# Kernel optimization log

Measured on AMD Instinct MI355X. Metric: run time of the kernel, lower is better.

Reference implementation:

```python
import jax, jax.numpy as jnp
import numpy as np

WS = 7        # window_size
HEADS = 4     # dim_in // dim_head = 256 // 64
DH = 64       # dim_head (for q/k)
SCALE = DH ** -0.5


def setup_inputs() -> dict:
    key = jax.random.key(0)
    k1, k2, k3 = jax.random.split(key, 3)
    x = jax.random.normal(k1, (32, 256, 56, 56), dtype=jnp.float32)
    qk_w = jax.random.normal(k2, (512, 256), dtype=jnp.float32) * 0.02  # 1x1 conv: (out_c, in_c)
    v_w = jax.random.normal(k3, (256, 256), dtype=jnp.float32) * 0.02
    return {"x": x, "qk_w": qk_w, "v_w": v_w}


def _forward(x, qk_w, v_w):
    B, C, H, W = x.shape
    pad_b = (WS - H % WS) % WS
    pad_r = (WS - W % WS) % WS
    x = jnp.pad(x, ((0, 0), (0, 0), (0, pad_b), (0, pad_r)))
    Hp, Wp = H + pad_b, W + pad_r
    n1, n2 = Hp // WS, Wp // WS

    # 1x1 convs (no bias): qk -> 2*C channels, v -> dim_mid channels with ReLU
    qk = jnp.einsum('bchw,oc->bohw', x, qk_w)
    v = jax.nn.relu(jnp.einsum('bchw,oc->bohw', x, v_w))

    # remote (dilated grid) partition: 'b c (h1 n1) (w1 n2) -> (b n1 n2) c h1 w1'
    def part_r(t):
        b, c = t.shape[:2]
        return t.reshape(b, c, WS, n1, WS, n2).transpose(0, 3, 5, 1, 2, 4).reshape(b * n1 * n2, c, WS, WS)

    def merge_r(t, b):
        c = t.shape[1]
        return t.reshape(b, n1, n2, c, WS, WS).transpose(0, 3, 4, 1, 5, 2).reshape(b, c, Hp, Wp)

    # close (contiguous window) partition: 'b c (n1 h1) (n2 w1) -> (b n1 n2) c h1 w1'
    def part_c(t):
        b, c = t.shape[:2]
        return t.reshape(b, c, n1, WS, n2, WS).transpose(0, 2, 4, 1, 3, 5).reshape(b * n1 * n2, c, WS, WS)

    def merge_c(t, b):
        c = t.shape[1]
        return t.reshape(b, n1, n2, c, WS, WS).transpose(0, 3, 1, 4, 2, 5).reshape(b, c, Hp, Wp)

    def win_attn(qk_win, v_win):
        # qk_win: (bw, 2*HEADS*DH, WS, WS); channel order is (qk, heads, dim_head)
        bw = qk_win.shape[0]
        N = WS * WS
        qkr = qk_win.reshape(bw, 2, HEADS, DH, N)
        q = qkr[:, 0].transpose(0, 1, 3, 2)  # (bw, heads, N, DH)
        k = qkr[:, 1].transpose(0, 1, 3, 2)
        dhv = v_win.shape[1] // HEADS
        vv = v_win.reshape(bw, HEADS, dhv, N).transpose(0, 1, 3, 2)  # (bw, heads, N, dhv)
        attn = jax.nn.softmax(jnp.einsum('bhnd,bhmd->bhnm', q, k) * SCALE, axis=-1)
        o = jnp.einsum('bhnm,bhmd->bhnd', attn, vv)
        return o.transpose(0, 1, 3, 2).reshape(bw, HEADS * dhv, WS, WS)

    o_remote = merge_r(win_attn(part_r(qk), part_r(v)), B)
    o_close = merge_c(win_attn(part_c(qk), part_c(v)), B)
    out = o_remote + o_close
    return out[:, :, :H, :W]


def reference(x, qk_w, v_w):
    return _forward(x, qk_w, v_w)
```

## Files before the change

### kernel.cpp

```cpp
#include <hip/hip_runtime.h>
#include <stdint.h>


typedef float f32x4 __attribute__((ext_vector_type(4)));
typedef __attribute__((ext_vector_type(8))) short short8;

union V16 { uint4 u; short8 s; unsigned short h[8]; };

typedef const __attribute__((address_space(1))) uint32_t* gp_t;
typedef __attribute__((address_space(3))) uint32_t* lp_t;

__device__ __forceinline__ void async16(const void* g, void* l) {
  __builtin_amdgcn_global_load_lds((gp_t)g, (lp_t)l, 16, 0, 0);
}

__device__ __forceinline__ unsigned short f2bf(float f) {
  union { float f; uint32_t u; } a; a.f = f;
  uint32_t u = a.u;
  return (unsigned short)((u + 0x7FFFu + ((u >> 16) & 1u)) >> 16);
}

__device__ __forceinline__ unsigned short f2bf_rhu(float f) {
  union { float f; uint32_t u; } a; a.f = f;
  return (unsigned short)((a.u + 0x8000u) >> 16);
}

__device__ __forceinline__ float bf2f(uint32_t bits_hi16) {
  union { uint32_t u; float f; } a; a.u = bits_hi16; return a.f;
}

__global__ __launch_bounds__(256) void k_wconv(const float* __restrict__ qk_w,
                                               const float* __restrict__ v_w,
                                               unsigned short* __restrict__ Wb) {
  int i = blockIdx.x * 256 + threadIdx.x;
  int o = i >> 5, gidx = i & 31;
  int c0 = gidx * 8;
  const float* src = (o < 512) ? (qk_w + o * 256 + c0) : (v_w + (o - 512) * 256 + c0);
  unsigned short vv[8];
#pragma unroll
  for (int j = 0; j < 8; j++) vv[j] = f2bf(src[j]);
  uint4 u;
  u.x = (uint32_t)vv[0] | ((uint32_t)vv[1] << 16);
  u.y = (uint32_t)vv[2] | ((uint32_t)vv[3] << 16);
  u.z = (uint32_t)vv[4] | ((uint32_t)vv[5] << 16);
  u.w = (uint32_t)vv[6] | ((uint32_t)vv[7] << 16);
  int kb = gidx >> 3, gg = gidx & 7;
  char* dst = (char*)Wb + (size_t)o * 512 + kb * 128 + ((gg ^ (o & 7)) << 4);
  *(uint4*)dst = u;
}

__global__ __launch_bounds__(256) void k_xpose(const float* __restrict__ x,
                                               unsigned short* __restrict__ xT) {
  const int t = threadIdx.x;
  const int p = blockIdx.x * 64 + (t >> 2);
  const int sub = t & 3;
  const int c0 = blockIdx.y * 32 + sub * 8;
  const int b = blockIdx.z;
  const float* xp = x + ((size_t)(b * 256 + c0)) * 3136 + p;
  unsigned short vv[8];
#pragma unroll
  for (int j = 0; j < 8; j++) vv[j] = f2bf(xp[(size_t)j * 3136]);
  uint4 u;
  u.x = (uint32_t)vv[0] | ((uint32_t)vv[1] << 16);
  u.y = (uint32_t)vv[2] | ((uint32_t)vv[3] << 16);
  u.z = (uint32_t)vv[4] | ((uint32_t)vv[5] << 16);
  u.w = (uint32_t)vv[6] | ((uint32_t)vv[7] << 16);
  const int g = (c0 >> 3) & 7;
  const int kb = c0 >> 6;
  char* dst = (char*)xT + ((size_t)(b * 3136 + p)) * 512 + kb * 128 + ((g ^ (p & 7)) << 4);
  *(uint4*)dst = u;
}

__global__ __launch_bounds__(256) void k_conv(const unsigned short* __restrict__ Wb,
                                              const unsigned short* __restrict__ xT,
                                              unsigned short* __restrict__ qkv) {
  __shared__ uint4 lds4[2048];
  char* ldsA = (char*)lds4;
  char* ldsB = (char*)lds4 + 16384;
  const int bi = blockIdx.x;
  const int xcd = bi & 7, g = bi >> 3;
  const int bgrp = g / 150;
  const int rem = g - bgrp * 150;
  const int b = xcd + 8 * bgrp;
  const int ot = rem / 25;
  const int pt = rem - ot * 25;
  const int p0 = pt * 128, o0 = ot * 128;
  const bool isv = (ot >= 4);
  const float qs = (ot < 2) ? 0.18033688011112042f : 1.0f;

  const int tid = threadIdx.x;
  const int lane = tid & 63, wave = tid >> 6;
  const int lid = lane & 15, quad = lane >> 4;
  const int m_off = (wave & 1) * 64, n_off = (wave >> 1) * 64;
  const int psub = lane >> 3, chunk = lane & 7;
  const size_t rowb = (size_t)(b * 3136 + p0);
  const char* xTb = (const char*)xT;
  const char* Wbb = (const char*)Wb;

  f32x4 acc[4][4];
#pragma unroll
  for (int mi = 0; mi < 4; mi++)
#pragma unroll
    for (int ni = 0; ni < 4; ni++) { f32x4 z = {0.f, 0.f, 0.f, 0.f}; acc[mi][ni] = z; }

  for (int kk = 0; kk < 256; kk += 64) {
#pragma unroll
    for (int r = 0; r < 4; r++) {
      int i = wave * 4 + r;
      const char* ga = Wbb + (size_t)(o0 + i * 8 + psub) * 512 + kk * 2 + chunk * 16;
      async16(ga, ldsA + i * 1024);
      const char* gb = xTb + (rowb + i * 8 + psub) * 512 + kk * 2 + chunk * 16;
      async16(gb, ldsB + i * 1024);
    }
    __syncthreads();

    V16 a[4][2], bf[4][2];
#pragma unroll
    for (int mi = 0; mi < 4; mi++) {
      int ro = m_off + mi * 16 + lid;
#pragma unroll
      for (int ks = 0; ks < 2; ks++) {
        int gl = ks * 4 + quad;
        a[mi][ks].u = *(const uint4*)(ldsA + ro * 128 + ((gl ^ (ro & 7)) << 4));
      }
    }
#pragma unroll
    for (int ni = 0; ni < 4; ni++) {
      int px = n_off + ni * 16 + lid;
#pragma unroll
      for (int ks = 0; ks < 2; ks++) {
        int gl = ks * 4 + quad;
        bf[ni][ks].u = *(const uint4*)(ldsB + px * 128 + ((gl ^ (px & 7)) << 4));
      }
    }
#pragma unroll
    for (int mi = 0; mi < 4; mi++)
#pragma unroll
      for (int ni = 0; ni < 4; ni++) {
        acc[mi][ni] = __builtin_amdgcn_mfma_f32_16x16x32_bf16(a[mi][0].s, bf[ni][0].s, acc[mi][ni], 0, 0, 0);
        acc[mi][ni] = __builtin_amdgcn_mfma_f32_16x16x32_bf16(a[mi][1].s, bf[ni][1].s, acc[mi][ni], 0, 0, 0);
      }
    __syncthreads();
  }

#pragma unroll
  for (int mi = 0; mi < 4; mi++) {
    int o = o0 + m_off + mi * 16 + quad * 4;
#pragma unroll
    for (int ni = 0; ni < 4; ni++) {
      int px = p0 + n_off + ni * 16 + lid;
      if (px < 3136) {
        f32x4 v = acc[mi][ni];
        v.x *= qs; v.y *= qs; v.z *= qs; v.w *= qs;
        if (isv) {
          v.x = fmaxf(v.x, 0.f); v.y = fmaxf(v.y, 0.f);
          v.z = fmaxf(v.z, 0.f); v.w = fmaxf(v.w, 0.f);
        }
        ushort4 u;
        u.x = f2bf(v.x); u.y = f2bf(v.y); u.z = f2bf(v.z); u.w = f2bf(v.w);
        *(ushort4*)(qkv + ((size_t)(b * 3136 + px)) * 768 + o) = u;
      }
    }
  }
}

__global__ __launch_bounds__(256) void k_attn(const unsigned short* __restrict__ qkv,
                                              unsigned short* __restrict__ oR,
                                              unsigned short* __restrict__ oC) {
  __shared__ uint4 smem4[2048];
  const int bi = blockIdx.x;
  const int xcd = bi & 7, g = bi >> 3;
  const int b = ((g >> 7) << 3) + xcd;
  const int rem = g & 127;
  const int part = rem >> 6;
  const int w = rem & 63;
  const int i1 = w >> 3, i2 = w & 7;
  const int off = part ? (i1 * 392 + i2 * 7) : (i1 * 56 + i2);
  const int sh  = part ? 56 : 448;
  const int sw  = part ? 1 : 8;

  const int lane = threadIdx.x & 63;
  const int head = threadIdx.x >> 6;
  const int lid = lane & 15, quad = lane >> 4;
  char* Pb = (char*)smem4 + head * 8192;
  const unsigned short* __restrict__ qkvb = qkv + (size_t)b * 3136 * 768;
  unsigned short* __restrict__ oSb = (part ? oC : oR) + (size_t)b * 3136 * 256;

  auto pix = [&](int t) -> int {
    int h1 = (t * 37) >> 8;
    int w1 = t - h1 * 7;
    return off + h1 * sh + w1 * sw;
  };

  V16 va[4][2];
#pragma unroll
  for (int ks = 0; ks < 2; ks++)
#pragma unroll
    for (int j = 0; j < 8; j++) {
      int key = ks * 32 + quad * 8 + j;
      int p = pix(min(key, 48));
      const unsigned short* vp = qkvb + p * 768 + 512 + head * 64 + lid;
#pragma unroll
      for (int mi = 0; mi < 4; mi++) va[mi][ks].h[j] = vp[mi * 16];
    }

  V16 qf[4][2], kf[4][2];
#pragma unroll
  for (int mi = 0; mi < 4; mi++) {
    int p = pix(min(mi * 16 + lid, 48));
    const unsigned short* qp = qkvb + p * 768 + head * 64;
#pragma unroll
    for (int ks = 0; ks < 2; ks++) qf[mi][ks].u = *(const uint4*)(qp + ks * 32 + quad * 8);
  }
#pragma unroll
  for (int ni = 0; ni < 4; ni++) {
    int p = pix(min(ni * 16 + lid, 48));
    const unsigned short* kp = qkvb + p * 768 + 256 + head * 64;
#pragma unroll
    for (int ks = 0; ks < 2; ks++) kf[ni][ks].u = *(const uint4*)(kp + ks * 32 + quad * 8);
  }

  f32x4 s[4][4];
#pragma unroll
  for (int mi = 0; mi < 4; mi++)
#pragma unroll
    for (int ni = 0; ni < 4; ni++) {
      f32x4 z = {0.f, 0.f, 0.f, 0.f};
      z = __builtin_amdgcn_mfma_f32_16x16x32_bf16(qf[mi][0].s, kf[ni][0].s, z, 0, 0, 0);
      z = __builtin_amdgcn_mfma_f32_16x16x32_bf16(qf[mi][1].s, kf[ni][1].s, z, 0, 0, 0);
      s[mi][ni] = z;
    }

  bool kvalid[4];
#pragma unroll
  for (int ni = 0; ni < 4; ni++) kvalid[ni] = (ni * 16 + lid) < 49;
  const int cl2 = (lid & 7) * 2;
#pragma unroll
  for (int mi = 0; mi < 4; mi++) {
#pragma unroll
    for (int r = 0; r < 4; r++) {
      int row = mi * 16 + quad * 4 + r;
      char* rp = Pb + row * 128;
      int rx = row & 7;
#pragma unroll
      for (int ni = 0; ni < 4; ni++) {
        float t = kvalid[ni] ? __builtin_amdgcn_exp2f(s[mi][ni][r]) : 0.f;
        int colgrp = ni * 2 + (lid >> 3);
        *(unsigned short*)(rp + (((colgrp ^ rx) << 4) + cl2)) = f2bf_rhu(t);
      }
    }
  }
  __syncthreads();

  V16 pt[4][2];
#pragma unroll
  for (int ni = 0; ni < 4; ni++) {
    int row = ni * 16 + lid;
#pragma unroll
    for (int ks = 0; ks < 2; ks++) {
      int gl = ks * 4 + quad;
      pt[ni][ks].u = *(const uint4*)(Pb + row * 128 + ((gl ^ (row & 7)) << 4));
    }
  }

  V16 ones;
#pragma unroll
  for (int j = 0; j < 8; j++) ones.h[j] = 0x3F80;
  float inv[4];
  int pq[4]; bool qv[4];
#pragma unroll
  for (int ni = 0; ni < 4; ni++) {
    f32x4 z = {0.f, 0.f, 0.f, 0.f};
    z = __builtin_amdgcn_mfma_f32_16x16x32_bf16(ones.s, pt[ni][0].s, z, 0, 0, 0);
    z = __builtin_amdgcn_mfma_f32_16x16x32_bf16(ones.s, pt[ni][1].s, z, 0, 0, 0);
    inv[ni] = __builtin_amdgcn_rcpf(z[0]);
    int q = ni * 16 + lid;
    qv[ni] = q < 49;
    pq[ni] = pix(qv[ni] ? q : 48);
  }

#pragma unroll
  for (int mi = 0; mi < 4; mi++) {
    f32x4 om[4];
#pragma unroll
    for (int ni = 0; ni < 4; ni++) {
      f32x4 z = {0.f, 0.f, 0.f, 0.f};
      z = __builtin_amdgcn_mfma_f32_16x16x32_bf16(va[mi][0].s, pt[ni][0].s, z, 0, 0, 0);
      z = __builtin_amdgcn_mfma_f32_16x16x32_bf16(va[mi][1].s, pt[ni][1].s, z, 0, 0, 0);
      om[ni] = z;
    }
#pragma unroll
    for (int ni = 0; ni < 4; ni++) {
      if (qv[ni]) {
        float iv = inv[ni];
        uint32_t lo = ((uint32_t)f2bf_rhu(om[ni][0] * iv)) | ((uint32_t)f2bf_rhu(om[ni][1] * iv) << 16);
        uint32_t hi = ((uint32_t)f2bf_rhu(om[ni][2] * iv)) | ((uint32_t)f2bf_rhu(om[ni][3] * iv) << 16);
        uint2 st; st.x = lo; st.y = hi;
        *(uint2*)(oSb + pq[ni] * 256 + head * 64 + mi * 16 + quad * 4) = st;
      }
    }
  }
}

__global__ __launch_bounds__(256) void k_merge(const unsigned short* __restrict__ oR,
                                               const unsigned short* __restrict__ oC,
                                               float* __restrict__ out) {
  __shared__ float lds[32 * 66];
  const int t = threadIdx.x;
  const int p0 = blockIdx.x * 64, c0 = blockIdx.y * 32, b = blockIdx.z;

  const int pl = t >> 2, cg = t & 3;
  size_t gi = ((size_t)(b * 3136 + p0 + pl)) * 256 + c0 + cg * 8;
  uint4 r1 = *(const uint4*)(oR + gi);
  uint4 r2 = *(const uint4*)(oC + gi);
  const uint32_t* a1 = (const uint32_t*)&r1;
  const uint32_t* a2 = (const uint32_t*)&r2;
#pragma unroll
  for (int j = 0; j < 4; j++) {
    float lo = bf2f(a1[j] << 16)         + bf2f(a2[j] << 16);
    float hi = bf2f(a1[j] & 0xFFFF0000u) + bf2f(a2[j] & 0xFFFF0000u);
    lds[(cg * 8 + j * 2)     * 66 + pl] = lo;
    lds[(cg * 8 + j * 2 + 1) * 66 + pl] = hi;
  }
  __syncthreads();

  const int lanec = t >> 4, pxl = (t & 15) * 4;
#pragma unroll
  for (int it = 0; it < 2; it++) {
    int c = it * 16 + lanec;
    float4 v;
    v.x = lds[c * 66 + pxl];
    v.y = lds[c * 66 + pxl + 1];
    v.z = lds[c * 66 + pxl + 2];
    v.w = lds[c * 66 + pxl + 3];
    *(float4*)(out + ((size_t)(b * 256 + c0 + c)) * 3136 + p0 + pxl) = v;
  }
}

extern "C" void kernel_launch(void* const* d_in, const int* in_sizes, int n_in,
                              void* d_out, int out_size, void* d_ws, size_t ws_size,
                              hipStream_t stream) {
  (void)in_sizes; (void)n_in; (void)out_size; (void)ws_size;
  const float* x    = (const float*)d_in[0];
  const float* qk_w = (const float*)d_in[1];
  const float* v_w  = (const float*)d_in[2];
  float* out = (float*)d_out;
  char* ws = (char*)d_ws;
  unsigned short* Wb  = (unsigned short*)ws;
  unsigned short* xT  = (unsigned short*)(ws + 393216);
  unsigned short* qkv = (unsigned short*)(ws + 51773440ull);
  unsigned short* oR  = xT;
  unsigned short* oC  = (unsigned short*)(ws + 205914112ull);

  hipLaunchKernelGGL(k_wconv, dim3(96), dim3(256), 0, stream, qk_w, v_w, Wb);
  hipLaunchKernelGGL(k_xpose, dim3(49, 8, 32), dim3(256), 0, stream, x, xT);
  hipLaunchKernelGGL(k_conv, dim3(4800), dim3(256), 0, stream, Wb, xT, qkv);
  hipLaunchKernelGGL(k_attn, dim3(4096), dim3(256), 0, stream, qkv, oR, oC);
  hipLaunchKernelGGL(k_merge, dim3(49, 8, 32), dim3(256), 0, stream, oR, oC, out);
}
```

Before: 367.9 us.

## Split attention into remote/close passes and fuse merge into the close pass

The single attention kernel becomes a template that runs twice: the remote pass writes a bf16 intermediate, and the close pass reads that intermediate, adds its own result and writes the fp32 NCHW output directly. This removes the separate merge kernel and the second bf16 intermediate buffer. The score MFMA operands are also swapped so each lane writes packed transposed P rows with 8-byte LDS stores instead of scalar shorts, and padding rows are zeroed without a per-element validity test. The fused output stores are strided by 3136 floats per channel, so they are less coalesced than the old merge kernel's float4 writes.

```diff
diff --git a/kernel.cpp b/kernel.cpp
--- a/kernel.cpp
+++ b/kernel.cpp
@@ -164,27 +164,26 @@
   }
 }
 
-__global__ __launch_bounds__(256) void k_attn(const unsigned short* __restrict__ qkv,
-                                              unsigned short* __restrict__ oR,
-                                              unsigned short* __restrict__ oC) {
+template <int PART, int FUSED>
+__global__ __launch_bounds__(256) void k_attn_t(const unsigned short* __restrict__ qkv,
+                                                const unsigned short* __restrict__ oPrev,
+                                                unsigned short* __restrict__ oDst,
+                                                float* __restrict__ out) {
   __shared__ uint4 smem4[2048];
   const int bi = blockIdx.x;
   const int xcd = bi & 7, g = bi >> 3;
-  const int b = ((g >> 7) << 3) + xcd;
-  const int rem = g & 127;
-  const int part = rem >> 6;
-  const int w = rem & 63;
+  const int b = ((g >> 6) << 3) + xcd;
+  const int w = g & 63;
   const int i1 = w >> 3, i2 = w & 7;
-  const int off = part ? (i1 * 392 + i2 * 7) : (i1 * 56 + i2);
-  const int sh  = part ? 56 : 448;
-  const int sw  = part ? 1 : 8;
+  const int off = PART ? (i1 * 392 + i2 * 7) : (i1 * 56 + i2);
+  const int sh  = PART ? 56 : 448;
+  const int sw  = PART ? 1 : 8;
 
   const int lane = threadIdx.x & 63;
   const int head = threadIdx.x >> 6;
   const int lid = lane & 15, quad = lane >> 4;
   char* Pb = (char*)smem4 + head * 8192;
   const unsigned short* __restrict__ qkvb = qkv + (size_t)b * 3136 * 768;
-  unsigned short* __restrict__ oSb = (part ? oC : oR) + (size_t)b * 3136 * 256;
 
   auto pix = [&](int t) -> int {
     int h1 = (t * 37) >> 8;
@@ -226,27 +225,31 @@
 #pragma unroll
     for (int ni = 0; ni < 4; ni++) {
       f32x4 z = {0.f, 0.f, 0.f, 0.f};
-      z = __builtin_amdgcn_mfma_f32_16x16x32_bf16(qf[mi][0].s, kf[ni][0].s, z, 0, 0, 0);
-      z = __builtin_amdgcn_mfma_f32_16x16x32_bf16(qf[mi][1].s, kf[ni][1].s, z, 0, 0, 0);
+      z = __builtin_amdgcn_mfma_f32_16x16x32_bf16(kf[mi][0].s, qf[ni][0].s, z, 0, 0, 0);
+      z = __builtin_amdgcn_mfma_f32_16x16x32_bf16(kf[mi][1].s, qf[ni][1].s, z, 0, 0, 0);
       s[mi][ni] = z;
     }
 
-  bool kvalid[4];
-#pragma unroll
-  for (int ni = 0; ni < 4; ni++) kvalid[ni] = (ni * 16 + lid) < 49;
-  const int cl2 = (lid & 7) * 2;
-#pragma unroll
-  for (int mi = 0; mi < 4; mi++) {
-#pragma unroll
-    for (int r = 0; r < 4; r++) {
-      int row = mi * 16 + quad * 4 + r;
-      char* rp = Pb + row * 128;
-      int rx = row & 7;
+  {
+    const int rx = lid & 7;
+    char* wbase = Pb + lid * 128 + (quad & 1) * 8;
+#pragma unroll
+    for (int mi = 0; mi < 4; mi++) {
+      const int swz = ((mi * 2 + (quad >> 1)) ^ rx) << 4;
 #pragma unroll
       for (int ni = 0; ni < 4; ni++) {
-        float t = kvalid[ni] ? __builtin_amdgcn_exp2f(s[mi][ni][r]) : 0.f;
-        int colgrp = ni * 2 + (lid >> 3);
-        *(unsigned short*)(rp + (((colgrp ^ rx) << 4) + cl2)) = f2bf_rhu(t);
+        uint32_t d0, d1;
+        if (mi < 3) {
+          d0 = (uint32_t)f2bf_rhu(__builtin_amdgcn_exp2f(s[mi][ni][0]))
+             | ((uint32_t)f2bf_rhu(__builtin_amdgcn_exp2f(s[mi][ni][1])) << 16);
+          d1 = (uint32_t)f2bf_rhu(__builtin_amdgcn_exp2f(s[mi][ni][2]))
+             | ((uint32_t)f2bf_rhu(__builtin_amdgcn_exp2f(s[mi][ni][3])) << 16);
+        } else {
+          d0 = quad ? 0u : (uint32_t)f2bf_rhu(__builtin_amdgcn_exp2f(s[3][ni][0]));
+          d1 = 0u;
+        }
+        uint2 st; st.x = d0; st.y = d1;
+        *(uint2*)(wbase + ni * 2048 + swz) = st;
       }
     }
   }
@@ -289,51 +292,39 @@
       z = __builtin_amdgcn_mfma_f32_16x16x32_bf16(va[mi][1].s, pt[ni][1].s, z, 0, 0, 0);
       om[ni] = z;
     }
-#pragma unroll
-    for (int ni = 0; ni < 4; ni++) {
-      if (qv[ni]) {
-        float iv = inv[ni];
-        uint32_t lo = ((uint32_t)f2bf_rhu(om[ni][0] * iv)) | ((uint32_t)f2bf_rhu(om[ni][1] * iv) << 16);
-        uint32_t hi = ((uint32_t)f2bf_rhu(om[ni][2] * iv)) | ((uint32_t)f2bf_rhu(om[ni][3] * iv) << 16);
-        uint2 st; st.x = lo; st.y = hi;
-        *(uint2*)(oSb + pq[ni] * 256 + head * 64 + mi * 16 + quad * 4) = st;
-      }
-    }
-  }
-}
-
-__global__ __launch_bounds__(256) void k_merge(const unsigned short* __restrict__ oR,
-                                               const unsigned short* __restrict__ oC,
-                                               float* __restrict__ out) {
-  __shared__ float lds[32 * 66];
-  const int t = threadIdx.x;
-  const int p0 = blockIdx.x * 64, c0 = blockIdx.y * 32, b = blockIdx.z;
-
-  const int pl = t >> 2, cg = t & 3;
-  size_t gi = ((size_t)(b * 3136 + p0 + pl)) * 256 + c0 + cg * 8;
-  uint4 r1 = *(const uint4*)(oR + gi);
-  uint4 r2 = *(const uint4*)(oC + gi);
-  const uint32_t* a1 = (const uint32_t*)&r1;
-  const uint32_t* a2 = (const uint32_t*)&r2;
-#pragma unroll
-  for (int j = 0; j < 4; j++) {
-    float lo = bf2f(a1[j] << 16)         + bf2f(a2[j] << 16);
-    float hi = bf2f(a1[j] & 0xFFFF0000u) + bf2f(a2[j] & 0xFFFF0000u);
-    lds[(cg * 8 + j * 2)     * 66 + pl] = lo;
-    lds[(cg * 8 + j * 2 + 1) * 66 + pl] = hi;
-  }
-  __syncthreads();
-
-  const int lanec = t >> 4, pxl = (t & 15) * 4;
-#pragma unroll
-  for (int it = 0; it < 2; it++) {
-    int c = it * 16 + lanec;
-    float4 v;
-    v.x = lds[c * 66 + pxl];
-    v.y = lds[c * 66 + pxl + 1];
-    v.z = lds[c * 66 + pxl + 2];
-    v.w = lds[c * 66 + pxl + 3];
-    *(float4*)(out + ((size_t)(b * 256 + c0 + c)) * 3136 + p0 + pxl) = v;
+    if constexpr (!FUSED) {
+      unsigned short* __restrict__ oSb = oDst + (size_t)b * 3136 * 256;
+#pragma unroll
+      for (int ni = 0; ni < 4; ni++) {
+        if (qv[ni]) {
+          float iv = inv[ni];
+          uint32_t lo = ((uint32_t)f2bf_rhu(om[ni][0] * iv)) | ((uint32_t)f2bf_rhu(om[ni][1] * iv) << 16);
+          uint32_t hi = ((uint32_t)f2bf_rhu(om[ni][2] * iv)) | ((uint32_t)f2bf_rhu(om[ni][3] * iv) << 16);
+          uint2 st; st.x = lo; st.y = hi;
+          *(uint2*)(oSb + pq[ni] * 256 + head * 64 + mi * 16 + quad * 4) = st;
+        }
+      }
+    } else {
+      const unsigned short* __restrict__ oPb = oPrev + (size_t)b * 3136 * 256;
+      float* __restrict__ outb = out + (size_t)b * 256 * 3136;
+      const int c0 = head * 64 + mi * 16 + quad * 4;
+#pragma unroll
+      for (int ni = 0; ni < 4; ni++) {
+        if (qv[ni]) {
+          float iv = inv[ni];
+          uint2 r = *(const uint2*)(oPb + pq[ni] * 256 + c0);
+          float o0 = om[ni][0] * iv + bf2f(r.x << 16);
+          float o1 = om[ni][1] * iv + bf2f(r.x & 0xFFFF0000u);
+          float o2 = om[ni][2] * iv + bf2f(r.y << 16);
+          float o3 = om[ni][3] * iv + bf2f(r.y & 0xFFFF0000u);
+          float* op = outb + (size_t)c0 * 3136 + pq[ni];
+          op[0]        = o0;
+          op[3136]     = o1;
+          op[2 * 3136] = o2;
+          op[3 * 3136] = o3;
+        }
+      }
+    }
   }
 }
 
@@ -350,11 +341,12 @@
   unsigned short* xT  = (unsigned short*)(ws + 393216);
   unsigned short* qkv = (unsigned short*)(ws + 51773440ull);
   unsigned short* oR  = xT;
-  unsigned short* oC  = (unsigned short*)(ws + 205914112ull);
 
   hipLaunchKernelGGL(k_wconv, dim3(96), dim3(256), 0, stream, qk_w, v_w, Wb);
   hipLaunchKernelGGL(k_xpose, dim3(49, 8, 32), dim3(256), 0, stream, x, xT);
   hipLaunchKernelGGL(k_conv, dim3(4800), dim3(256), 0, stream, Wb, xT, qkv);
-  hipLaunchKernelGGL(k_attn, dim3(4096), dim3(256), 0, stream, qkv, oR, oC);
-  hipLaunchKernelGGL(k_merge, dim3(49, 8, 32), dim3(256), 0, stream, oR, oC, out);
-}
+  hipLaunchKernelGGL(HIP_KERNEL_NAME(k_attn_t<0, 0>), dim3(2048), dim3(256), 0, stream,
+                     qkv, (const unsigned short*)nullptr, oR, (float*)nullptr);
+  hipLaunchKernelGGL(HIP_KERNEL_NAME(k_attn_t<1, 1>), dim3(2048), dim3(256), 0, stream,
+                     qkv, (const unsigned short*)oR, (unsigned short*)nullptr, out);
+}
```

Measured after the change: 367.2 us. No clear change (-0.2%).
